# Kernel optimization log

Hardware: AMD Instinct MI355X
Metric: run time of the kernel (lower is better)

Reference implementation:

```python
import jax, jax.numpy as jnp
import numpy as np

N = 4096
STEPS = 32


def setup_inputs() -> dict:
    key = jax.random.key(0)
    k0, k1, k2, k3 = jax.random.split(key, 4)
    x = jax.random.normal(k0, (N, 2), dtype=jnp.float32) * 0.02
    raw_S = jax.random.normal(k1, (N, N), dtype=jnp.float32) * 0.1
    raw_phase = jax.random.normal(k2, (N, N), dtype=jnp.float32) * 0.1
    # raw_r initialized at logit(p_r0=0.2) in the original module
    init_logit = float(np.log(0.2 / 0.8))
    raw_r = jnp.full((N, N), init_logit, dtype=jnp.float32)
    mask = (jax.random.uniform(k3, (N, N)) < 0.1).astype(jnp.float32)
    A_mask = jnp.maximum(mask, jnp.eye(N, dtype=jnp.float32))
    G_gate = jnp.ones((N, N), dtype=jnp.float32)
    omega = jnp.float32(0.1)
    return {"x": x, "raw_S": raw_S, "raw_phase": raw_phase, "raw_r": raw_r,
            "A_mask": A_mask, "G_gate": G_gate, "omega": omega, "steps": STEPS}


def reference(x, raw_S, raw_phase, raw_r, A_mask, G_gate, omega, steps):
    # Effective amplitude adjacency (beta=0, no do-interventions): same at every step
    S = jnp.tanh(raw_S)
    r = jax.nn.sigmoid(raw_r)
    Aamp = A_mask * G_gate * S * r  # [N, N]

    def step(xc, t):
        theta = raw_phase + omega * t          # [N, N] time-varying phase
        c = jnp.cos(theta)
        s = jnp.sin(theta)
        xr = xc[:, 0]  # [N]
        xi = xc[:, 1]  # [N]
        out_r = (Aamp * c) @ xr - (Aamp * s) @ xi
        out_i = (Aamp * s) @ xr + (Aamp * c) @ xi
        x_next = jnp.stack([jnp.tanh(out_r), jnp.tanh(out_i)], axis=-1)  # [N, 2]
        return x_next, x_next

    ts = jnp.arange(steps, dtype=x.dtype)
    _, traj = jax.lax.scan(step, x, ts)
    return jnp.concatenate([x[None], traj], axis=0)  # [steps+1, N, 2]
```

## Files before the change

kernel.cpp:

```cpp
#include <hip/hip_runtime.h>
#include <cstdint>
#include <cstddef>

#define N 4096
#define STEPS 32
#define PADW 640

__device__ __forceinline__ float bf16lo_to_f(uint32_t u) {
    return __uint_as_float(u << 16);
}
__device__ __forceinline__ float bf16hi_to_f(uint32_t u) {
    return __uint_as_float(u & 0xFFFF0000u);
}
__device__ __forceinline__ uint32_t f_to_bf16bits(float f) {
    uint32_t u = __float_as_uint(f);
    return (u + 0x7FFFu + ((u >> 16) & 1u)) >> 16;
}
__device__ __forceinline__ float fast_tanh(float x) {
    float e = __expf(2.0f * x);
    return (e - 1.0f) * __builtin_amdgcn_rcpf(e + 1.0f);
}
__device__ __forceinline__ float fast_sigmoid(float x) {
    return __builtin_amdgcn_rcpf(1.0f + __expf(-x));
}


__global__ __launch_bounds__(256) void fill_sparse_kernel(
    const float* __restrict__ raw_S,
    const float* __restrict__ raw_phase,
    const float* __restrict__ raw_r,
    const float* __restrict__ A_mask,
    const float* __restrict__ G_gate,
    uint16_t* __restrict__ col16,
    uint16_t* __restrict__ pc16,
    uint16_t* __restrict__ ps16)
{
    const int wave = threadIdx.x >> 6;
    const int lane = threadIdx.x & 63;
    const int row  = blockIdx.x * 4 + wave;
    const size_t rbase = (size_t)row * N;
    const size_t pbase = (size_t)row * PADW;

    int base = 0;
#pragma unroll 2
    for (int j = 0; j < N / 64; j++) {
        int c = j * 64 + lane;
        float m  = A_mask[rbase + c];
        float g  = G_gate[rbase + c];
        float sv = raw_S[rbase + c];
        float rv = raw_r[rbase + c];
        float pv = raw_phase[rbase + c];
        bool p = (m != 0.0f);
        unsigned long long bal = __ballot(p);

        float S  = fast_tanh(sv);
        float rr = fast_sigmoid(rv);
        float amp = m * g * S * rr;
        uint32_t pc = f_to_bf16bits(amp * __cosf(pv));
        uint32_t ps = f_to_bf16bits(amp * __sinf(pv));

        if (p) {
            int prefix = __popcll(bal & ((1ull << lane) - 1ull));
            int idx = base + prefix;
            if (idx < PADW) {
                col16[pbase + idx] = (uint16_t)c;
                pc16[pbase + idx]  = (uint16_t)pc;
                ps16[pbase + idx]  = (uint16_t)ps;
            }
        }
        base += (int)__popcll(bal);
    }
    if (base > PADW) base = PADW;
    for (int i = base + lane; i < PADW; i += 64) {
        col16[pbase + i] = 0;
        pc16[pbase + i]  = 0;
        ps16[pbase + i]  = 0;
    }
}

__global__ __launch_bounds__(256) void step_sparse_kernel(
    const uint16_t* __restrict__ col16,
    const uint16_t* __restrict__ pc16,
    const uint16_t* __restrict__ ps16,
    const float* __restrict__ x_in,
    float* __restrict__ x_out,
    const float* __restrict__ omega_ptr,
    int t)
{
    __shared__ float xs[2 * N];
    const int tid = threadIdx.x;
    {
        const float4* src = (const float4*)x_in;
        float4* dst = (float4*)xs;
#pragma unroll
        for (int i = 0; i < 8; i++)
            dst[tid + 256 * i] = src[tid + 256 * i];
    }
    __syncthreads();

    const int wave = tid >> 6;
    const int lane = tid & 63;
    float theta = omega_ptr[0] * (float)t;
    float st, ct;
    __sincosf(theta, &st, &ct);

#pragma unroll
    for (int rr = 0; rr < 2; rr++) {
        const int row = blockIdx.x * 8 + rr * 4 + wave;
        const uint32_t* colp = (const uint32_t*)(col16 + (size_t)row * PADW);
        const uint32_t* pcp  = (const uint32_t*)(pc16  + (size_t)row * PADW);
        const uint32_t* psp  = (const uint32_t*)(ps16  + (size_t)row * PADW);
        float are = 0.0f, aim = 0.0f;
#pragma unroll
        for (int j = 0; j < PADW / 128; j++) {
            uint32_t cc  = colp[j * 64 + lane];
            uint32_t pc2 = pcp[j * 64 + lane];
            uint32_t ps2 = psp[j * 64 + lane];
            int c0 = (int)(cc & 0xFFFFu), c1 = (int)(cc >> 16);
            float2 x0 = *(const float2*)(xs + 2 * c0);
            float2 x1 = *(const float2*)(xs + 2 * c1);
            float pc0 = bf16lo_to_f(pc2), pc1 = bf16hi_to_f(pc2);
            float ps0 = bf16lo_to_f(ps2), ps1 = bf16hi_to_f(ps2);
            are = fmaf(pc0, x0.x, are); are = fmaf(-ps0, x0.y, are);
            aim = fmaf(ps0, x0.x, aim); aim = fmaf(pc0, x0.y, aim);
            are = fmaf(pc1, x1.x, are); are = fmaf(-ps1, x1.y, are);
            aim = fmaf(ps1, x1.x, aim); aim = fmaf(pc1, x1.y, aim);
        }
#pragma unroll
        for (int off = 32; off; off >>= 1) {
            are += __shfl_down(are, off);
            aim += __shfl_down(aim, off);
        }
        if (lane == 0) {
            float ore = ct * are - st * aim;
            float oim = st * are + ct * aim;
            *(float2*)(x_out + 2 * row) =
                make_float2(fast_tanh(ore), fast_tanh(oim));
        }
    }
}


__global__ __launch_bounds__(256) void precompute_kernel(
    const float* __restrict__ raw_phase,
    const float* __restrict__ raw_r,
    const float* __restrict__ A_mask,
    const float* __restrict__ G_gate,
    const float* raw_S_in,
    float* dst)
{
    int idx = (blockIdx.x * 256 + threadIdx.x) * 4;
    float4 s4 = *(const float4*)(raw_S_in + idx);
    float4 p4 = *(const float4*)(raw_phase + idx);
    float4 r4 = *(const float4*)(raw_r + idx);
    float4 m4 = *(const float4*)(A_mask + idx);
    float4 g4 = *(const float4*)(G_gate + idx);
    float sv[4] = {s4.x, s4.y, s4.z, s4.w};
    float pv[4] = {p4.x, p4.y, p4.z, p4.w};
    float rv[4] = {r4.x, r4.y, r4.z, r4.w};
    float mv[4] = {m4.x, m4.y, m4.z, m4.w};
    float gv[4] = {g4.x, g4.y, g4.z, g4.w};
    float ov[4];
#pragma unroll
    for (int k = 0; k < 4; k++) {
        float S = fast_tanh(sv[k]);
        float r = fast_sigmoid(rv[k]);
        float amp = mv[k] * gv[k] * S * r;
        uint32_t pc = f_to_bf16bits(amp * __cosf(pv[k]));
        uint32_t ps = f_to_bf16bits(amp * __sinf(pv[k]));
        ov[k] = __uint_as_float((ps << 16) | pc);
    }
    *(float4*)(dst + idx) = make_float4(ov[0], ov[1], ov[2], ov[3]);
}

__global__ __launch_bounds__(512, 8) void step_kernel(
    const float* __restrict__ Mpacked_f,
    const float* __restrict__ x_in,
    float* __restrict__ x_out,
    const float* __restrict__ omega_ptr,
    int t)
{
    const int tid  = threadIdx.x;
    const int wave = tid >> 6;
    const int lane = tid & 63;
    const int row0 = blockIdx.x * 4;
    const uint32_t* M = (const uint32_t*)Mpacked_f;
    const int cbase = (wave << 9) + (lane << 2);
    float xr[8], xi[8];
#pragma unroll
    for (int s = 0; s < 2; s++) {
        int j = cbase + (s << 8);
        float4 a = *(const float4*)(x_in + 2 * j);
        float4 b = *(const float4*)(x_in + 2 * j + 4);
        xr[4*s+0]=a.x; xi[4*s+0]=a.y; xr[4*s+1]=a.z; xi[4*s+1]=a.w;
        xr[4*s+2]=b.x; xi[4*s+2]=b.y; xr[4*s+3]=b.z; xi[4*s+3]=b.w;
    }
    __shared__ float part[8][4][2];
#pragma unroll
    for (int r = 0; r < 4; r++) {
        const uint32_t* Mrow = M + (size_t)(row0 + r) * N + cbase;
        float are = 0.0f, aim = 0.0f;
#pragma unroll
        for (int s = 0; s < 2; s++) {
            uint4 m = *(const uint4*)(Mrow + (s << 8));
            uint32_t mm[4] = {m.x, m.y, m.z, m.w};
#pragma unroll
            for (int k = 0; k < 4; k++) {
                float pc = bf16lo_to_f(mm[k]);
                float ps = bf16hi_to_f(mm[k]);
                float xre = xr[4*s+k], xim = xi[4*s+k];
                are = fmaf(pc, xre, are); are = fmaf(-ps, xim, are);
                aim = fmaf(ps, xre, aim); aim = fmaf(pc, xim, aim);
            }
        }
#pragma unroll
        for (int off = 32; off; off >>= 1) {
            are += __shfl_down(are, off);
            aim += __shfl_down(aim, off);
        }
        if (lane == 0) { part[wave][r][0] = are; part[wave][r][1] = aim; }
    }
    __syncthreads();
    if (tid < 4) {
        float U = 0.0f, V = 0.0f;
#pragma unroll
        for (int w = 0; w < 8; w++) { U += part[w][tid][0]; V += part[w][tid][1]; }
        float theta = omega_ptr[0] * (float)t;
        float stv, ctv;
        __sincosf(theta, &stv, &ctv);
        float ore = ctv * U - stv * V;
        float oim = stv * U + ctv * V;
        int row = row0 + tid;
        x_out[2*row+0] = fast_tanh(ore);
        x_out[2*row+1] = fast_tanh(oim);
    }
}


extern "C" void kernel_launch(void* const* d_in, const int* in_sizes, int n_in,
                              void* d_out, int out_size, void* d_ws, size_t ws_size,
                              hipStream_t stream) {
    const float* x         = (const float*)d_in[0];
    float*       raw_S     = (float*)d_in[1];
    const float* raw_phase = (const float*)d_in[2];
    const float* raw_r     = (const float*)d_in[3];
    const float* A_mask    = (const float*)d_in[4];
    const float* G_gate    = (const float*)d_in[5];
    const float* omega     = (const float*)d_in[6];
    float* out = (float*)d_out;

    hipMemcpyAsync(out, x, (size_t)N * 2 * sizeof(float),
                   hipMemcpyDeviceToDevice, stream);

    const size_t plane = (size_t)N * PADW * sizeof(uint16_t);
    if (ws_size >= 3 * plane) {
        uint16_t* col16 = (uint16_t*)d_ws;
        uint16_t* pc16  = col16 + (size_t)N * PADW;
        uint16_t* ps16  = pc16 + (size_t)N * PADW;

        fill_sparse_kernel<<<dim3(N / 4), dim3(256), 0, stream>>>(
            raw_S, raw_phase, raw_r, A_mask, G_gate, col16, pc16, ps16);

        for (int t = 0; t < STEPS; t++) {
            step_sparse_kernel<<<dim3(N / 8), dim3(256), 0, stream>>>(
                col16, pc16, ps16,
                out + (size_t)t * N * 2,
                out + (size_t)(t + 1) * N * 2,
                omega, t);
        }
    } else {
        float* packed = raw_S;
        precompute_kernel<<<dim3(N * (N / 1024)), dim3(256), 0, stream>>>(
            raw_phase, raw_r, A_mask, G_gate, raw_S, packed);
        for (int t = 0; t < STEPS; t++) {
            step_kernel<<<dim3(N / 4), dim3(512), 0, stream>>>(
                packed,
                out + (size_t)t * N * 2,
                out + (size_t)(t + 1) * N * 2,
                omega, t);
        }
    }
}
```

Before: 450.3 us.

## Interleave cos/sin values, vectorize fill loads with prefetch, one row per wave

The fill kernel now reads its five input matrices with float4 loads and prefetches the next chunk, and packs the bf16 cos and sin amplitudes into a single 32-bit word per nonzero. The step kernel reads the packed values as uint2, so each iteration issues one value load instead of two. It also processes one row per wave with twice as many blocks, which costs an extra reload of x into shared memory per block. The fill kernel's input loads (about 320MB of fp32 reads) are meant to be the dominant cost. The extra per-block staging of x is the trade-off.

```diff
diff --git a/kernel.cpp b/kernel.cpp
--- a/kernel.cpp
+++ b/kernel.cpp
@@ -32,8 +32,7 @@
     const float* __restrict__ A_mask,
     const float* __restrict__ G_gate,
     uint16_t* __restrict__ col16,
-    uint16_t* __restrict__ pc16,
-    uint16_t* __restrict__ ps16)
+    uint32_t* __restrict__ val32)
 {
     const int wave = threadIdx.x >> 6;
     const int lane = threadIdx.x & 63;
@@ -42,46 +41,64 @@
     const size_t pbase = (size_t)row * PADW;
 
     int base = 0;
+    size_t off0 = rbase + lane * 4;
+    float4 m4 = *(const float4*)(A_mask + off0);
+    float4 g4 = *(const float4*)(G_gate + off0);
+    float4 s4 = *(const float4*)(raw_S + off0);
+    float4 r4 = *(const float4*)(raw_r + off0);
+    float4 p4 = *(const float4*)(raw_phase + off0);
+
 #pragma unroll 2
-    for (int j = 0; j < N / 64; j++) {
-        int c = j * 64 + lane;
-        float m  = A_mask[rbase + c];
-        float g  = G_gate[rbase + c];
-        float sv = raw_S[rbase + c];
-        float rv = raw_r[rbase + c];
-        float pv = raw_phase[rbase + c];
-        bool p = (m != 0.0f);
-        unsigned long long bal = __ballot(p);
-
-        float S  = fast_tanh(sv);
-        float rr = fast_sigmoid(rv);
-        float amp = m * g * S * rr;
-        uint32_t pc = f_to_bf16bits(amp * __cosf(pv));
-        uint32_t ps = f_to_bf16bits(amp * __sinf(pv));
-
-        if (p) {
-            int prefix = __popcll(bal & ((1ull << lane) - 1ull));
-            int idx = base + prefix;
-            if (idx < PADW) {
-                col16[pbase + idx] = (uint16_t)c;
-                pc16[pbase + idx]  = (uint16_t)pc;
-                ps16[pbase + idx]  = (uint16_t)ps;
+    for (int j = 0; j < N / 256; j++) {
+        float mv[4] = {m4.x, m4.y, m4.z, m4.w};
+        float gv[4] = {g4.x, g4.y, g4.z, g4.w};
+        float sv[4] = {s4.x, s4.y, s4.z, s4.w};
+        float rv[4] = {r4.x, r4.y, r4.z, r4.w};
+        float pv[4] = {p4.x, p4.y, p4.z, p4.w};
+        if (j < N / 256 - 1) {
+            size_t off = rbase + (j + 1) * 256 + lane * 4;
+            m4 = *(const float4*)(A_mask + off);
+            g4 = *(const float4*)(G_gate + off);
+            s4 = *(const float4*)(raw_S + off);
+            r4 = *(const float4*)(raw_r + off);
+            p4 = *(const float4*)(raw_phase + off);
+        }
+
+        uint32_t pk[4];
+        bool pr[4];
+#pragma unroll
+        for (int k = 0; k < 4; k++) {
+            pr[k] = (mv[k] != 0.0f);
+            float S  = fast_tanh(sv[k]);
+            float rr = fast_sigmoid(rv[k]);
+            float amp = mv[k] * gv[k] * S * rr;
+            uint32_t pc = f_to_bf16bits(amp * __cosf(pv[k]));
+            uint32_t ps = f_to_bf16bits(amp * __sinf(pv[k]));
+            pk[k] = (ps << 16) | pc;
+        }
+#pragma unroll
+        for (int k = 0; k < 4; k++) {
+            unsigned long long bal = __ballot(pr[k]);
+            if (pr[k]) {
+                int idx = base + __popcll(bal & ((1ull << lane) - 1ull));
+                if (idx < PADW) {
+                    col16[pbase + idx] = (uint16_t)(j * 256 + lane * 4 + k);
+                    val32[pbase + idx] = pk[k];
+                }
             }
-        }
-        base += (int)__popcll(bal);
+            base += (int)__popcll(bal);
+        }
     }
     if (base > PADW) base = PADW;
     for (int i = base + lane; i < PADW; i += 64) {
         col16[pbase + i] = 0;
-        pc16[pbase + i]  = 0;
-        ps16[pbase + i]  = 0;
+        val32[pbase + i] = 0;
     }
 }
 
 __global__ __launch_bounds__(256) void step_sparse_kernel(
     const uint16_t* __restrict__ col16,
-    const uint16_t* __restrict__ pc16,
-    const uint16_t* __restrict__ ps16,
+    const uint32_t* __restrict__ val32,
     const float* __restrict__ x_in,
     float* __restrict__ x_out,
     const float* __restrict__ omega_ptr,
@@ -100,43 +117,39 @@
 
     const int wave = tid >> 6;
     const int lane = tid & 63;
-    float theta = omega_ptr[0] * (float)t;
-    float st, ct;
-    __sincosf(theta, &st, &ct);
-
-#pragma unroll
-    for (int rr = 0; rr < 2; rr++) {
-        const int row = blockIdx.x * 8 + rr * 4 + wave;
-        const uint32_t* colp = (const uint32_t*)(col16 + (size_t)row * PADW);
-        const uint32_t* pcp  = (const uint32_t*)(pc16  + (size_t)row * PADW);
-        const uint32_t* psp  = (const uint32_t*)(ps16  + (size_t)row * PADW);
-        float are = 0.0f, aim = 0.0f;
-#pragma unroll
-        for (int j = 0; j < PADW / 128; j++) {
-            uint32_t cc  = colp[j * 64 + lane];
-            uint32_t pc2 = pcp[j * 64 + lane];
-            uint32_t ps2 = psp[j * 64 + lane];
-            int c0 = (int)(cc & 0xFFFFu), c1 = (int)(cc >> 16);
-            float2 x0 = *(const float2*)(xs + 2 * c0);
-            float2 x1 = *(const float2*)(xs + 2 * c1);
-            float pc0 = bf16lo_to_f(pc2), pc1 = bf16hi_to_f(pc2);
-            float ps0 = bf16lo_to_f(ps2), ps1 = bf16hi_to_f(ps2);
-            are = fmaf(pc0, x0.x, are); are = fmaf(-ps0, x0.y, are);
-            aim = fmaf(ps0, x0.x, aim); aim = fmaf(pc0, x0.y, aim);
-            are = fmaf(pc1, x1.x, are); are = fmaf(-ps1, x1.y, are);
-            aim = fmaf(ps1, x1.x, aim); aim = fmaf(pc1, x1.y, aim);
-        }
-#pragma unroll
-        for (int off = 32; off; off >>= 1) {
-            are += __shfl_down(are, off);
-            aim += __shfl_down(aim, off);
-        }
-        if (lane == 0) {
-            float ore = ct * are - st * aim;
-            float oim = st * are + ct * aim;
-            *(float2*)(x_out + 2 * row) =
-                make_float2(fast_tanh(ore), fast_tanh(oim));
-        }
+    const int row = blockIdx.x * 4 + wave;
+
+    const uint32_t* colp = (const uint32_t*)(col16 + (size_t)row * PADW);
+    const uint2*    valp = (const uint2*)(val32 + (size_t)row * PADW);
+
+    float are = 0.0f, aim = 0.0f;
+#pragma unroll
+    for (int j = 0; j < PADW / 128; j++) {
+        uint32_t cc = colp[j * 64 + lane];
+        uint2    vv = valp[j * 64 + lane];
+        int c0 = (int)(cc & 0xFFFFu), c1 = (int)(cc >> 16);
+        float2 x0 = *(const float2*)(xs + 2 * c0);
+        float2 x1 = *(const float2*)(xs + 2 * c1);
+        float pc0 = bf16lo_to_f(vv.x), ps0 = bf16hi_to_f(vv.x);
+        float pc1 = bf16lo_to_f(vv.y), ps1 = bf16hi_to_f(vv.y);
+        are = fmaf(pc0, x0.x, are); are = fmaf(-ps0, x0.y, are);
+        aim = fmaf(ps0, x0.x, aim); aim = fmaf(pc0, x0.y, aim);
+        are = fmaf(pc1, x1.x, are); are = fmaf(-ps1, x1.y, are);
+        aim = fmaf(ps1, x1.x, aim); aim = fmaf(pc1, x1.y, aim);
+    }
+#pragma unroll
+    for (int off = 32; off; off >>= 1) {
+        are += __shfl_down(are, off);
+        aim += __shfl_down(aim, off);
+    }
+    if (lane == 0) {
+        float theta = omega_ptr[0] * (float)t;
+        float st, ct;
+        __sincosf(theta, &st, &ct);
+        float ore = ct * are - st * aim;
+        float oim = st * are + ct * aim;
+        *(float2*)(x_out + 2 * row) =
+            make_float2(fast_tanh(ore), fast_tanh(oim));
     }
 }
 
@@ -252,18 +265,18 @@
     hipMemcpyAsync(out, x, (size_t)N * 2 * sizeof(float),
                    hipMemcpyDeviceToDevice, stream);
 
-    const size_t plane = (size_t)N * PADW * sizeof(uint16_t);
-    if (ws_size >= 3 * plane) {
+    const size_t colBytes = (size_t)N * PADW * sizeof(uint16_t);
+    const size_t valBytes = (size_t)N * PADW * sizeof(uint32_t);
+    if (ws_size >= colBytes + valBytes) {
         uint16_t* col16 = (uint16_t*)d_ws;
-        uint16_t* pc16  = col16 + (size_t)N * PADW;
-        uint16_t* ps16  = pc16 + (size_t)N * PADW;
+        uint32_t* val32 = (uint32_t*)((char*)d_ws + colBytes);
 
         fill_sparse_kernel<<<dim3(N / 4), dim3(256), 0, stream>>>(
-            raw_S, raw_phase, raw_r, A_mask, G_gate, col16, pc16, ps16);
+            raw_S, raw_phase, raw_r, A_mask, G_gate, col16, val32);
 
         for (int t = 0; t < STEPS; t++) {
-            step_sparse_kernel<<<dim3(N / 8), dim3(256), 0, stream>>>(
-                col16, pc16, ps16,
+            step_sparse_kernel<<<dim3(N / 4), dim3(256), 0, stream>>>(
+                col16, val32,
                 out + (size_t)t * N * 2,
                 out + (size_t)(t + 1) * N * 2,
                 omega, t);
```

Measured after the change: 453.5 us. About the same (+0.7%).
